# Kernel optimization log

Hardware: AMD Instinct MI355X
Metric: run time of the kernel (lower is better)

## Reference

```python
import jax, jax.numpy as jnp
import numpy as np

N_NODES = 100000


def sage_conv(x, edge_index, Wl, bl, Wr):
    # PyG SAGEConv (aggr='mean', root_weight=True):
    #   out_i = lin_l(mean_{j in N(i)} x_j) + lin_r(x_i)
    src, dst = edge_index[0], edge_index[1]
    msgs = x[src]  # [E, C] gather of source-node features
    summed = jax.ops.segment_sum(msgs, dst, num_segments=N_NODES)
    deg = jax.ops.segment_sum(jnp.ones((edge_index.shape[1],), x.dtype), dst,
                              num_segments=N_NODES)
    mean = summed / jnp.maximum(deg, 1.0)[:, None]  # zero rows stay zero
    return mean @ Wl.T + bl + x @ Wr.T


def setup_inputs() -> dict:
    key = jax.random.key(0)
    ks = jax.random.split(key, 12)
    IN, HID, OUT = 128, 128, 64
    E, P = 1600000, 200000
    x = jax.random.normal(ks[0], (N_NODES, IN), jnp.float32)
    edge_index = jax.random.randint(ks[1], (2, E), 0, N_NODES)
    edge_label_index = jax.random.randint(ks[2], (2, P), 0, N_NODES)
    s1 = 1.0 / np.sqrt(IN)
    s2 = 1.0 / np.sqrt(HID)
    s3 = 1.0 / np.sqrt(2 * OUT)
    return {
        "x": x,
        "edge_index": edge_index,
        "edge_label_index": edge_label_index,
        "Wl1": jax.random.uniform(ks[3], (HID, IN), jnp.float32, -s1, s1),
        "bl1": jnp.zeros((HID,), jnp.float32),
        "Wr1": jax.random.uniform(ks[4], (HID, IN), jnp.float32, -s1, s1),
        "Wl2": jax.random.uniform(ks[5], (OUT, HID), jnp.float32, -s2, s2),
        "bl2": jnp.zeros((OUT,), jnp.float32),
        "Wr2": jax.random.uniform(ks[6], (OUT, HID), jnp.float32, -s2, s2),
        "Wdec": jax.random.uniform(ks[7], (1, 2 * OUT), jnp.float32, -s3, s3),
        "bdec": jax.random.uniform(ks[8], (1,), jnp.float32, -s3, s3),
    }


def reference(x, edge_index, edge_label_index, Wl1, bl1, Wr1, Wl2, bl2, Wr2,
              Wdec, bdec):
    # encode: SAGEConv -> relu -> (dropout p=0) -> SAGEConv
    h = jax.nn.relu(sage_conv(x, edge_index, Wl1, bl1, Wr1))
    z = sage_conv(h, edge_index, Wl2, bl2, Wr2)
    # decode: gather endpoint embeddings, concat, linear -> [P]
    feats = jnp.concatenate([z[edge_label_index[0]], z[edge_label_index[1]]],
                            axis=-1)
    return (feats @ Wdec.T + bdec).reshape(-1)
```

## Files before the change

### kernel.cpp

```cpp
#include <hip/hip_runtime.h>

#define NN 100000
#define NBUK ((NN + 255) / 256)
#define BCAP 5120

typedef unsigned short u16;
typedef unsigned int u32;
typedef __attribute__((ext_vector_type(8))) short short8v;
typedef __attribute__((ext_vector_type(4))) float float4v;

__device__ __forceinline__ u32 f2bf_rne(float f) {
    u32 x = __float_as_uint(f);
    return (x + 0x7fffu + ((x >> 16) & 1u)) >> 16;
}
__device__ __forceinline__ float bf2f(u32 u) {
    return __uint_as_float(u << 16);
}
__device__ __forceinline__ uint4 pack8u(const float4& a, const float4& b) {
    uint4 u;
    u.x = f2bf_rne(a.x) | (f2bf_rne(a.y) << 16);
    u.y = f2bf_rne(a.z) | (f2bf_rne(a.w) << 16);
    u.z = f2bf_rne(b.x) | (f2bf_rne(b.y) << 16);
    u.w = f2bf_rne(b.z) | (f2bf_rne(b.w) << 16);
    return u;
}

__global__ void zero_buckets_kernel(int* __restrict__ p) {
    int i = threadIdx.x;
    if (i < NBUK) p[i] = 0;
}

__global__ __launch_bounds__(256) void partition_kernel(const int* __restrict__ edges,
                                                        int* __restrict__ bucketCnt,
                                                        int* __restrict__ bucketed, int E) {
    __shared__ int h[NBUK];
    __shared__ int base[NBUK];
    for (int i = threadIdx.x; i < NBUK; i += 256) h[i] = 0;
    __syncthreads();
    int b0 = blockIdx.x * 4096;
    for (int k = threadIdx.x; k < 4096; k += 256) {
        int e = b0 + k;
        if (e < E) atomicAdd(&h[edges[E + e] >> 8], 1);
    }
    __syncthreads();
    for (int i = threadIdx.x; i < NBUK; i += 256) {
        int c = h[i];
        base[i] = c ? (i * BCAP + atomicAdd(&bucketCnt[i], c)) : 0;
        h[i] = 0;
    }
    __syncthreads();
    for (int k = threadIdx.x; k < 4096; k += 256) {
        int e = b0 + k;
        if (e < E) {
            int d = edges[E + e];
            int b = d >> 8;
            int off = atomicAdd(&h[b], 1);
            bucketed[base[b] + off] = edges[e] | ((d & 255) << 20);
        }
    }
}

__global__ __launch_bounds__(256) void bucket_sort_kernel(const int* __restrict__ bucketed,
                                                          const int* __restrict__ bucketCnt,
                                                          int* __restrict__ rowStart,
                                                          int* __restrict__ cnt,
                                                          int* __restrict__ sortedSrc, int N) {
    __shared__ int h[256];
    __shared__ int pos[256];
    int b = blockIdx.x;
    int tid = threadIdx.x;
    int start = b * BCAP, end = start + bucketCnt[b];
    h[tid] = 0;
    __syncthreads();
    for (int k = start + tid; k < end; k += 256) atomicAdd(&h[bucketed[k] >> 20], 1);
    __syncthreads();
    int v = h[tid];
    pos[tid] = v;
    __syncthreads();
    for (int off = 1; off < 256; off <<= 1) {
        int t = (tid >= off) ? pos[tid - off] : 0;
        __syncthreads();
        pos[tid] += t;
        __syncthreads();
    }
    int excl = start + pos[tid] - v;
    int node = (b << 8) + tid;
    if (node < N) {
        rowStart[node] = excl;
        cnt[node] = v;
    }
    h[tid] = excl;
    __syncthreads();
    for (int k = start + tid; k < end; k += 256) {
        int entry = bucketed[k];
        int p = atomicAdd(&h[entry >> 20], 1);
        sortedSrc[p] = entry & 0xFFFFF;
    }
}

template <bool XF32>
__global__ __launch_bounds__(256, 2) void gemm_mfma_kernel(
    const void* __restrict__ Xv, const float* __restrict__ Wa,
    const float* __restrict__ Wb, int CHALF,
    u16* __restrict__ Ob, int OSTRIDE, int N)
{
    __shared__ u16 As[128 * 128];

    const int tid = threadIdx.x;
    const int w = tid >> 6;
    const int l = tid & 63;
    const int l15 = l & 15;
    const int lhi = l >> 4;
    const int rowBase = blockIdx.x * 128;
    const int cBase = blockIdx.y * 128;
    char* asb = reinterpret_cast<char*>(As);

#pragma unroll
    for (int i = 0; i < 8; ++i) {
        int q = tid + i * 256;
        int r = q >> 4, c = q & 15;
        int gr = rowBase + r;
        uint4 pk = make_uint4(0u, 0u, 0u, 0u);
        if (gr < N) {
            if (XF32) {
                const float* xf = (const float*)Xv + (size_t)gr * 128 + c * 8;
                float4 f0 = *reinterpret_cast<const float4*>(xf);
                float4 f1 = *reinterpret_cast<const float4*>(xf + 4);
                pk = pack8u(f0, f1);
            } else {
                pk = *reinterpret_cast<const uint4*>((const u16*)Xv + (size_t)gr * 128 + c * 8);
            }
        }
        *reinterpret_cast<uint4*>(asb + r * 256 + ((c * 16) ^ ((r & 7) << 4))) = pk;
    }

    short8v bfrag[2][4];
#pragma unroll
    for (int nj = 0; nj < 2; ++nj) {
        int c = cBase + w * 32 + nj * 16 + l15;
        const float* wr = (c < CHALF) ? (Wa + (size_t)c * 128)
                                      : (Wb + (size_t)(c - CHALF) * 128);
#pragma unroll
        for (int kk = 0; kk < 4; ++kk) {
            float4 f0 = *reinterpret_cast<const float4*>(wr + kk * 32 + lhi * 8);
            float4 f1 = *reinterpret_cast<const float4*>(wr + kk * 32 + lhi * 8 + 4);
            uint4 pk = pack8u(f0, f1);
            union { uint4 u; short8v s; } cv; cv.u = pk;
            bfrag[nj][kk] = cv.s;
        }
    }

    __syncthreads();

    float4v acc[8][2];
    const float4v az = {0.f, 0.f, 0.f, 0.f};
#pragma unroll
    for (int mi = 0; mi < 8; ++mi) { acc[mi][0] = az; acc[mi][1] = az; }

#pragma unroll
    for (int kk = 0; kk < 4; ++kk) {
#pragma unroll
        for (int mi = 0; mi < 8; ++mi) {
            int r = mi * 16 + l15;
            short8v a = *reinterpret_cast<const short8v*>(
                asb + r * 256 + ((kk * 64 + lhi * 16) ^ ((r & 7) << 4)));
            acc[mi][0] = __builtin_amdgcn_mfma_f32_16x16x32_bf16(a, bfrag[0][kk], acc[mi][0], 0, 0, 0);
            acc[mi][1] = __builtin_amdgcn_mfma_f32_16x16x32_bf16(a, bfrag[1][kk], acc[mi][1], 0, 0, 0);
        }
    }

    __syncthreads();
#pragma unroll
    for (int mi = 0; mi < 8; ++mi) {
#pragma unroll
        for (int nj = 0; nj < 2; ++nj) {
            int cc = w * 32 + nj * 16 + l15;
#pragma unroll
            for (int j = 0; j < 4; ++j) {
                int r = mi * 16 + lhi * 4 + j;
                *reinterpret_cast<u16*>(asb + r * 256 + ((cc * 2) ^ ((r & 7) << 4)))
                    = (u16)f2bf_rne(acc[mi][nj][j]);
            }
        }
    }
    __syncthreads();
#pragma unroll
    for (int i = 0; i < 8; ++i) {
        int q = tid + i * 256;
        int r = q >> 4, c = q & 15;
        int gr = rowBase + r;
        if (gr < N) {
            uint4 v = *reinterpret_cast<const uint4*>(
                asb + r * 256 + ((c * 16) ^ ((r & 7) << 4)));
            *reinterpret_cast<uint4*>(&Ob[(size_t)gr * OSTRIDE + cBase + c * 8]) = v;
        }
    }
}

template <int C, bool RELU>
__global__ __launch_bounds__(256) void agg_combine_kernel(
    const u16* __restrict__ T, int tStride,
    const u16* __restrict__ R,
    const int* __restrict__ sortedSrc, const int* __restrict__ rowStart,
    const int* __restrict__ cnt, const float* __restrict__ bias,
    u16* __restrict__ outB, int N)
{
    constexpr int TPN = C / 8;
    constexpr int NPB = 256 / TPN;
    int n = blockIdx.x * NPB + threadIdx.x / TPN;
    int c = threadIdx.x % TPN;
    if (n >= N) return;
    int start = rowStart[n];
    int m = cnt[n];
    const int* __restrict__ ep = sortedSrc + start;
    const u16* __restrict__ tp = T + c * 8;

    float a0 = 0.f, a1 = 0.f, a2 = 0.f, a3 = 0.f;
    float a4 = 0.f, a5 = 0.f, a6 = 0.f, a7 = 0.f;
    int k = 0;
    for (; k + 8 <= m; k += 8) {
        int s[8];
        uint4 v[8];
#pragma unroll
        for (int u = 0; u < 8; ++u) s[u] = ep[k + u];
#pragma unroll
        for (int u = 0; u < 8; ++u)
            v[u] = *reinterpret_cast<const uint4*>(&tp[(size_t)s[u] * tStride]);
#pragma unroll
        for (int h = 0; h < 2; ++h) {
            const uint4& w0 = v[h * 4 + 0]; const uint4& w1 = v[h * 4 + 1];
            const uint4& w2 = v[h * 4 + 2]; const uint4& w3 = v[h * 4 + 3];
            a0 += bf2f(w0.x & 0xffffu) + bf2f(w1.x & 0xffffu) + bf2f(w2.x & 0xffffu) + bf2f(w3.x & 0xffffu);
            a1 += bf2f(w0.x >> 16) + bf2f(w1.x >> 16) + bf2f(w2.x >> 16) + bf2f(w3.x >> 16);
            a2 += bf2f(w0.y & 0xffffu) + bf2f(w1.y & 0xffffu) + bf2f(w2.y & 0xffffu) + bf2f(w3.y & 0xffffu);
            a3 += bf2f(w0.y >> 16) + bf2f(w1.y >> 16) + bf2f(w2.y >> 16) + bf2f(w3.y >> 16);
            a4 += bf2f(w0.z & 0xffffu) + bf2f(w1.z & 0xffffu) + bf2f(w2.z & 0xffffu) + bf2f(w3.z & 0xffffu);
            a5 += bf2f(w0.z >> 16) + bf2f(w1.z >> 16) + bf2f(w2.z >> 16) + bf2f(w3.z >> 16);
            a6 += bf2f(w0.w & 0xffffu) + bf2f(w1.w & 0xffffu) + bf2f(w2.w & 0xffffu) + bf2f(w3.w & 0xffffu);
            a7 += bf2f(w0.w >> 16) + bf2f(w1.w >> 16) + bf2f(w2.w >> 16) + bf2f(w3.w >> 16);
        }
    }
    for (; k + 4 <= m; k += 4) {
        int s0 = ep[k], s1 = ep[k + 1], s2 = ep[k + 2], s3 = ep[k + 3];
        uint4 w0 = *reinterpret_cast<const uint4*>(&tp[(size_t)s0 * tStride]);
        uint4 w1 = *reinterpret_cast<const uint4*>(&tp[(size_t)s1 * tStride]);
        uint4 w2 = *reinterpret_cast<const uint4*>(&tp[(size_t)s2 * tStride]);
        uint4 w3 = *reinterpret_cast<const uint4*>(&tp[(size_t)s3 * tStride]);
        a0 += bf2f(w0.x & 0xffffu) + bf2f(w1.x & 0xffffu) + bf2f(w2.x & 0xffffu) + bf2f(w3.x & 0xffffu);
        a1 += bf2f(w0.x >> 16) + bf2f(w1.x >> 16) + bf2f(w2.x >> 16) + bf2f(w3.x >> 16);
        a2 += bf2f(w0.y & 0xffffu) + bf2f(w1.y & 0xffffu) + bf2f(w2.y & 0xffffu) + bf2f(w3.y & 0xffffu);
        a3 += bf2f(w0.y >> 16) + bf2f(w1.y >> 16) + bf2f(w2.y >> 16) + bf2f(w3.y >> 16);
        a4 += bf2f(w0.z & 0xffffu) + bf2f(w1.z & 0xffffu) + bf2f(w2.z & 0xffffu) + bf2f(w3.z & 0xffffu);
        a5 += bf2f(w0.z >> 16) + bf2f(w1.z >> 16) + bf2f(w2.z >> 16) + bf2f(w3.z >> 16);
        a6 += bf2f(w0.w & 0xffffu) + bf2f(w1.w & 0xffffu) + bf2f(w2.w & 0xffffu) + bf2f(w3.w & 0xffffu);
        a7 += bf2f(w0.w >> 16) + bf2f(w1.w >> 16) + bf2f(w2.w >> 16) + bf2f(w3.w >> 16);
    }
    for (; k < m; ++k) {
        uint4 v = *reinterpret_cast<const uint4*>(&tp[(size_t)ep[k] * tStride]);
        a0 += bf2f(v.x & 0xffffu); a1 += bf2f(v.x >> 16);
        a2 += bf2f(v.y & 0xffffu); a3 += bf2f(v.y >> 16);
        a4 += bf2f(v.z & 0xffffu); a5 += bf2f(v.z >> 16);
        a6 += bf2f(v.w & 0xffffu); a7 += bf2f(v.w >> 16);
    }
    float inv = 1.0f / fmaxf((float)m, 1.0f);
    uint4 rv = *reinterpret_cast<const uint4*>(&R[(size_t)n * tStride + c * 8]);
    float o0 = fmaf(a0, inv, bias[c * 8 + 0]) + bf2f(rv.x & 0xffffu);
    float o1 = fmaf(a1, inv, bias[c * 8 + 1]) + bf2f(rv.x >> 16);
    float o2 = fmaf(a2, inv, bias[c * 8 + 2]) + bf2f(rv.y & 0xffffu);
    float o3 = fmaf(a3, inv, bias[c * 8 + 3]) + bf2f(rv.y >> 16);
    float o4 = fmaf(a4, inv, bias[c * 8 + 4]) + bf2f(rv.z & 0xffffu);
    float o5 = fmaf(a5, inv, bias[c * 8 + 5]) + bf2f(rv.z >> 16);
    float o6 = fmaf(a6, inv, bias[c * 8 + 6]) + bf2f(rv.w & 0xffffu);
    float o7 = fmaf(a7, inv, bias[c * 8 + 7]) + bf2f(rv.w >> 16);
    if (RELU) {
        o0 = fmaxf(o0, 0.f); o1 = fmaxf(o1, 0.f);
        o2 = fmaxf(o2, 0.f); o3 = fmaxf(o3, 0.f);
        o4 = fmaxf(o4, 0.f); o5 = fmaxf(o5, 0.f);
        o6 = fmaxf(o6, 0.f); o7 = fmaxf(o7, 0.f);
    }
    uint4 o;
    o.x = f2bf_rne(o0) | (f2bf_rne(o1) << 16);
    o.y = f2bf_rne(o2) | (f2bf_rne(o3) << 16);
    o.z = f2bf_rne(o4) | (f2bf_rne(o5) << 16);
    o.w = f2bf_rne(o6) | (f2bf_rne(o7) << 16);
    *reinterpret_cast<uint4*>(&outB[(size_t)n * C + c * 8]) = o;
}

__global__ __launch_bounds__(256) void decode_kernel(
    const u16* __restrict__ z, const int* __restrict__ eli,
    const float* __restrict__ Wdec, const float* __restrict__ bdec,
    float* __restrict__ out, int P)
{
    int t = blockIdx.x * 256 + threadIdx.x;
    int p = t >> 6;
    int lane = t & 63;
    if (p >= P) return;
    int a = eli[p];
    int b = eli[P + p];
    float acc = bf2f(z[(size_t)a * 64 + lane]) * Wdec[lane]
              + bf2f(z[(size_t)b * 64 + lane]) * Wdec[64 + lane];
    for (int off = 32; off; off >>= 1) acc += __shfl_down(acc, off);
    if (lane == 0) out[p] = acc + bdec[0];
}

extern "C" void kernel_launch(void* const* d_in, const int* in_sizes, int n_in,
                              void* d_out, int out_size, void* d_ws, size_t ws_size,
                              hipStream_t stream) {
    const float* x    = (const float*)d_in[0];
    const int*   ei   = (const int*)d_in[1];
    const int*   eli  = (const int*)d_in[2];
    const float* Wl1  = (const float*)d_in[3];
    const float* bl1  = (const float*)d_in[4];
    const float* Wr1  = (const float*)d_in[5];
    const float* Wl2  = (const float*)d_in[6];
    const float* bl2  = (const float*)d_in[7];
    const float* Wr2  = (const float*)d_in[8];
    const float* Wdec = (const float*)d_in[9];
    const float* bdec = (const float*)d_in[10];
    float* out = (float*)d_out;

    const int N = NN;
    const int E = in_sizes[1] / 2;
    const int P = in_sizes[2] / 2;
    const int EB = (E + 4095) / 4096;

    char* wp = (char*)d_ws;
    u16* obf = (u16*)wp;  wp += (size_t)N * 256 * 2;
    u16* hbf = (u16*)wp;  wp += (size_t)N * 128 * 2;
    u16* zb  = (u16*)wp;  wp += (size_t)N * 64 * 2;
    int* bucketCnt = (int*)wp;
    int* rowStart  = bucketCnt + NBUK;
    int* cnt       = rowStart + N;
    int* bucketed  = cnt + N;
    int* sortedSrc = bucketed + NBUK * BCAP;

    zero_buckets_kernel<<<1, 512, 0, stream>>>(bucketCnt);
    partition_kernel<<<EB, 256, 0, stream>>>(ei, bucketCnt, bucketed, E);
    bucket_sort_kernel<<<NBUK, 256, 0, stream>>>(bucketed, bucketCnt, rowStart, cnt, sortedSrc, N);

    {
        dim3 grid((N + 127) / 128, 2);
        gemm_mfma_kernel<true><<<grid, 256, 0, stream>>>(x, Wl1, Wr1, 128, obf, 256, N);
    }
    agg_combine_kernel<128, true><<<(N + 15) / 16, 256, 0, stream>>>(
        obf, 256, obf + 128, sortedSrc, rowStart, cnt, bl1, hbf, N);

    {
        dim3 grid((N + 127) / 128, 1);
        gemm_mfma_kernel<false><<<grid, 256, 0, stream>>>(hbf, Wl2, Wr2, 64, obf, 128, N);
    }
    agg_combine_kernel<64, false><<<(N + 31) / 32, 256, 0, stream>>>(
        obf, 128, obf + 64, sortedSrc, rowStart, cnt, bl2, zb, N);

    decode_kernel<<<(P + 3) / 4, 256, 0, stream>>>(zb, eli, Wdec, bdec, out, P);
}
```

Before: 233.4 us.

## Fold decoder into second aggregation and loop column blocks inside GEMM

The second-layer aggregation now projects each node's z straight onto the two halves of the decoder weights and stores a per-node float2 (u, v), so decode only gathers two floats per label pair instead of two 64-wide bf16 rows. The first-layer GEMM loops over both 128-column blocks inside one workgroup, reusing the staged A tile instead of launching a second grid column that reloads and reconverts x. It adds a separate LDS output buffer for this. The zero-init kernel is replaced by hipMemsetAsync, and the 4-wide remainder loop in aggregation is dropped. The trade-offs are more LDS per block (lower occupancy) and a different bf16 rounding point, since z is no longer stored as bf16 before the decoder.

After: 210.9 us. -9.6%, faster.

```diff
diff --git a/kernel.cpp b/kernel.cpp
--- a/kernel.cpp
+++ b/kernel.cpp
@@ -23,11 +23,6 @@
     u.z = f2bf_rne(b.x) | (f2bf_rne(b.y) << 16);
     u.w = f2bf_rne(b.z) | (f2bf_rne(b.w) << 16);
     return u;
-}
-
-__global__ void zero_buckets_kernel(int* __restrict__ p) {
-    int i = threadIdx.x;
-    if (i < NBUK) p[i] = 0;
 }
 
 __global__ __launch_bounds__(256) void partition_kernel(const int* __restrict__ edges,
@@ -98,13 +93,14 @@
     }
 }
 
-template <bool XF32>
+template <bool XF32, int NCB>
 __global__ __launch_bounds__(256, 2) void gemm_mfma_kernel(
     const void* __restrict__ Xv, const float* __restrict__ Wa,
     const float* __restrict__ Wb, int CHALF,
     u16* __restrict__ Ob, int OSTRIDE, int N)
 {
     __shared__ u16 As[128 * 128];
+    __shared__ u16 Cs[128 * 128];
 
     const int tid = threadIdx.x;
     const int w = tid >> 6;
@@ -112,8 +108,8 @@
     const int l15 = l & 15;
     const int lhi = l >> 4;
     const int rowBase = blockIdx.x * 128;
-    const int cBase = blockIdx.y * 128;
     char* asb = reinterpret_cast<char*>(As);
+    char* csb = reinterpret_cast<char*>(Cs);
 
 #pragma unroll
     for (int i = 0; i < 8; ++i) {
@@ -133,66 +129,68 @@
         }
         *reinterpret_cast<uint4*>(asb + r * 256 + ((c * 16) ^ ((r & 7) << 4))) = pk;
     }
-
-    short8v bfrag[2][4];
-#pragma unroll
-    for (int nj = 0; nj < 2; ++nj) {
-        int c = cBase + w * 32 + nj * 16 + l15;
-        const float* wr = (c < CHALF) ? (Wa + (size_t)c * 128)
-                                      : (Wb + (size_t)(c - CHALF) * 128);
+    __syncthreads();
+
+    for (int cb = 0; cb < NCB; ++cb) {
+        const int cBase = cb * 128;
+        short8v bfrag[2][4];
+#pragma unroll
+        for (int nj = 0; nj < 2; ++nj) {
+            int c = cBase + w * 32 + nj * 16 + l15;
+            const float* wr = (c < CHALF) ? (Wa + (size_t)c * 128)
+                                          : (Wb + (size_t)(c - CHALF) * 128);
+#pragma unroll
+            for (int kk = 0; kk < 4; ++kk) {
+                float4 f0 = *reinterpret_cast<const float4*>(wr + kk * 32 + lhi * 8);
+                float4 f1 = *reinterpret_cast<const float4*>(wr + kk * 32 + lhi * 8 + 4);
+                uint4 pk = pack8u(f0, f1);
+                union { uint4 u; short8v s; } cv; cv.u = pk;
+                bfrag[nj][kk] = cv.s;
+            }
+        }
+
+        float4v acc[8][2];
+        const float4v az = {0.f, 0.f, 0.f, 0.f};
+#pragma unroll
+        for (int mi = 0; mi < 8; ++mi) { acc[mi][0] = az; acc[mi][1] = az; }
+
 #pragma unroll
         for (int kk = 0; kk < 4; ++kk) {
-            float4 f0 = *reinterpret_cast<const float4*>(wr + kk * 32 + lhi * 8);
-            float4 f1 = *reinterpret_cast<const float4*>(wr + kk * 32 + lhi * 8 + 4);
-            uint4 pk = pack8u(f0, f1);
-            union { uint4 u; short8v s; } cv; cv.u = pk;
-            bfrag[nj][kk] = cv.s;
-        }
-    }
-
-    __syncthreads();
-
-    float4v acc[8][2];
-    const float4v az = {0.f, 0.f, 0.f, 0.f};
-#pragma unroll
-    for (int mi = 0; mi < 8; ++mi) { acc[mi][0] = az; acc[mi][1] = az; }
-
-#pragma unroll
-    for (int kk = 0; kk < 4; ++kk) {
+#pragma unroll
+            for (int mi = 0; mi < 8; ++mi) {
+                int r = mi * 16 + l15;
+                short8v a = *reinterpret_cast<const short8v*>(
+                    asb + r * 256 + ((kk * 64 + lhi * 16) ^ ((r & 7) << 4)));
+                acc[mi][0] = __builtin_amdgcn_mfma_f32_16x16x32_bf16(a, bfrag[0][kk], acc[mi][0], 0, 0, 0);
+                acc[mi][1] = __builtin_amdgcn_mfma_f32_16x16x32_bf16(a, bfrag[1][kk], acc[mi][1], 0, 0, 0);
+            }
+        }
+
+        if (cb) __syncthreads();
 #pragma unroll
         for (int mi = 0; mi < 8; ++mi) {
-            int r = mi * 16 + l15;
-            short8v a = *reinterpret_cast<const short8v*>(
-                asb + r * 256 + ((kk * 64 + lhi * 16) ^ ((r & 7) << 4)));
-            acc[mi][0] = __builtin_amdgcn_mfma_f32_16x16x32_bf16(a, bfrag[0][kk], acc[mi][0], 0, 0, 0);
-            acc[mi][1] = __builtin_amdgcn_mfma_f32_16x16x32_bf16(a, bfrag[1][kk], acc[mi][1], 0, 0, 0);
-        }
-    }
-
-    __syncthreads();
-#pragma unroll
-    for (int mi = 0; mi < 8; ++mi) {
-#pragma unroll
-        for (int nj = 0; nj < 2; ++nj) {
-            int cc = w * 32 + nj * 16 + l15;
-#pragma unroll
-            for (int j = 0; j < 4; ++j) {
-                int r = mi * 16 + lhi * 4 + j;
-                *reinterpret_cast<u16*>(asb + r * 256 + ((cc * 2) ^ ((r & 7) << 4)))
-                    = (u16)f2bf_rne(acc[mi][nj][j]);
+#pragma unroll
+            for (int nj = 0; nj < 2; ++nj) {
+                int cc = w * 32 + nj * 16 + l15;
+#pragma unroll
+                for (int j = 0; j < 4; ++j) {
+                    int r = mi * 16 + lhi * 4 + j;
+                    *reinterpret_cast<u16*>(csb + r * 256 + ((cc * 2) ^ ((r & 7) << 4)))
+                        = (u16)f2bf_rne(acc[mi][nj][j]);
+                }
             }
         }
-    }
-    __syncthreads();
-#pragma unroll
-    for (int i = 0; i < 8; ++i) {
-        int q = tid + i * 256;
-        int r = q >> 4, c = q & 15;
-        int gr = rowBase + r;
-        if (gr < N) {
-            uint4 v = *reinterpret_cast<const uint4*>(
-                asb + r * 256 + ((c * 16) ^ ((r & 7) << 4)));
-            *reinterpret_cast<uint4*>(&Ob[(size_t)gr * OSTRIDE + cBase + c * 8]) = v;
+        __syncthreads();
+#pragma unroll
+        for (int i = 0; i < 8; ++i) {
+            int q = tid + i * 256;
+            int r = q >> 4, c = q & 15;
+            int gr = rowBase + r;
+            if (gr < N) {
+                uint4 v = *reinterpret_cast<const uint4*>(
+                    csb + r * 256 + ((c * 16) ^ ((r & 7) << 4)));
+                *reinterpret_cast<uint4*>(&Ob[(size_t)gr * OSTRIDE + cBase + c * 8]) = v;
+            }
         }
     }
 }
@@ -240,21 +238,6 @@
             a7 += bf2f(w0.w >> 16) + bf2f(w1.w >> 16) + bf2f(w2.w >> 16) + bf2f(w3.w >> 16);
         }
     }
-    for (; k + 4 <= m; k += 4) {
-        int s0 = ep[k], s1 = ep[k + 1], s2 = ep[k + 2], s3 = ep[k + 3];
-        uint4 w0 = *reinterpret_cast<const uint4*>(&tp[(size_t)s0 * tStride]);
-        uint4 w1 = *reinterpret_cast<const uint4*>(&tp[(size_t)s1 * tStride]);
-        uint4 w2 = *reinterpret_cast<const uint4*>(&tp[(size_t)s2 * tStride]);
-        uint4 w3 = *reinterpret_cast<const uint4*>(&tp[(size_t)s3 * tStride]);
-        a0 += bf2f(w0.x & 0xffffu) + bf2f(w1.x & 0xffffu) + bf2f(w2.x & 0xffffu) + bf2f(w3.x & 0xffffu);
-        a1 += bf2f(w0.x >> 16) + bf2f(w1.x >> 16) + bf2f(w2.x >> 16) + bf2f(w3.x >> 16);
-        a2 += bf2f(w0.y & 0xffffu) + bf2f(w1.y & 0xffffu) + bf2f(w2.y & 0xffffu) + bf2f(w3.y & 0xffffu);
-        a3 += bf2f(w0.y >> 16) + bf2f(w1.y >> 16) + bf2f(w2.y >> 16) + bf2f(w3.y >> 16);
-        a4 += bf2f(w0.z & 0xffffu) + bf2f(w1.z & 0xffffu) + bf2f(w2.z & 0xffffu) + bf2f(w3.z & 0xffffu);
-        a5 += bf2f(w0.z >> 16) + bf2f(w1.z >> 16) + bf2f(w2.z >> 16) + bf2f(w3.z >> 16);
-        a6 += bf2f(w0.w & 0xffffu) + bf2f(w1.w & 0xffffu) + bf2f(w2.w & 0xffffu) + bf2f(w3.w & 0xffffu);
-        a7 += bf2f(w0.w >> 16) + bf2f(w1.w >> 16) + bf2f(w2.w >> 16) + bf2f(w3.w >> 16);
-    }
     for (; k < m; ++k) {
         uint4 v = *reinterpret_cast<const uint4*>(&tp[(size_t)ep[k] * tStride]);
         a0 += bf2f(v.x & 0xffffu); a1 += bf2f(v.x >> 16);
@@ -286,21 +269,89 @@
     *reinterpret_cast<uint4*>(&outB[(size_t)n * C + c * 8]) = o;
 }
 
+__global__ __launch_bounds__(256) void agg_uv_kernel(
+    const u16* __restrict__ T, int tStride,
+    const u16* __restrict__ R,
+    const int* __restrict__ sortedSrc, const int* __restrict__ rowStart,
+    const int* __restrict__ cnt, const float* __restrict__ bias,
+    const float* __restrict__ Wdec, float2* __restrict__ uv, int N)
+{
+    constexpr int TPN = 8;
+    constexpr int NPB = 256 / TPN;
+    int n = blockIdx.x * NPB + threadIdx.x / TPN;
+    int c = threadIdx.x % TPN;
+    if (n >= N) return;
+    int start = rowStart[n];
+    int m = cnt[n];
+    const int* __restrict__ ep = sortedSrc + start;
+    const u16* __restrict__ tp = T + c * 8;
+
+    float a0 = 0.f, a1 = 0.f, a2 = 0.f, a3 = 0.f;
+    float a4 = 0.f, a5 = 0.f, a6 = 0.f, a7 = 0.f;
+    int k = 0;
+    for (; k + 8 <= m; k += 8) {
+        int s[8];
+        uint4 v[8];
+#pragma unroll
+        for (int u = 0; u < 8; ++u) s[u] = ep[k + u];
+#pragma unroll
+        for (int u = 0; u < 8; ++u)
+            v[u] = *reinterpret_cast<const uint4*>(&tp[(size_t)s[u] * tStride]);
+#pragma unroll
+        for (int h = 0; h < 2; ++h) {
+            const uint4& w0 = v[h * 4 + 0]; const uint4& w1 = v[h * 4 + 1];
+            const uint4& w2 = v[h * 4 + 2]; const uint4& w3 = v[h * 4 + 3];
+            a0 += bf2f(w0.x & 0xffffu) + bf2f(w1.x & 0xffffu) + bf2f(w2.x & 0xffffu) + bf2f(w3.x & 0xffffu);
+            a1 += bf2f(w0.x >> 16) + bf2f(w1.x >> 16) + bf2f(w2.x >> 16) + bf2f(w3.x >> 16);
+            a2 += bf2f(w0.y & 0xffffu) + bf2f(w1.y & 0xffffu) + bf2f(w2.y & 0xffffu) + bf2f(w3.y & 0xffffu);
+            a3 += bf2f(w0.y >> 16) + bf2f(w1.y >> 16) + bf2f(w2.y >> 16) + bf2f(w3.y >> 16);
+            a4 += bf2f(w0.z & 0xffffu) + bf2f(w1.z & 0xffffu) + bf2f(w2.z & 0xffffu) + bf2f(w3.z & 0xffffu);
+            a5 += bf2f(w0.z >> 16) + bf2f(w1.z >> 16) + bf2f(w2.z >> 16) + bf2f(w3.z >> 16);
+            a6 += bf2f(w0.w & 0xffffu) + bf2f(w1.w & 0xffffu) + bf2f(w2.w & 0xffffu) + bf2f(w3.w & 0xffffu);
+            a7 += bf2f(w0.w >> 16) + bf2f(w1.w >> 16) + bf2f(w2.w >> 16) + bf2f(w3.w >> 16);
+        }
+    }
+    for (; k < m; ++k) {
+        uint4 v = *reinterpret_cast<const uint4*>(&tp[(size_t)ep[k] * tStride]);
+        a0 += bf2f(v.x & 0xffffu); a1 += bf2f(v.x >> 16);
+        a2 += bf2f(v.y & 0xffffu); a3 += bf2f(v.y >> 16);
+        a4 += bf2f(v.z & 0xffffu); a5 += bf2f(v.z >> 16);
+        a6 += bf2f(v.w & 0xffffu); a7 += bf2f(v.w >> 16);
+    }
+    float inv = 1.0f / fmaxf((float)m, 1.0f);
+    uint4 rv = *reinterpret_cast<const uint4*>(&R[(size_t)n * tStride + c * 8]);
+    float z0 = fmaf(a0, inv, bias[c * 8 + 0]) + bf2f(rv.x & 0xffffu);
+    float z1 = fmaf(a1, inv, bias[c * 8 + 1]) + bf2f(rv.x >> 16);
+    float z2 = fmaf(a2, inv, bias[c * 8 + 2]) + bf2f(rv.y & 0xffffu);
+    float z3 = fmaf(a3, inv, bias[c * 8 + 3]) + bf2f(rv.y >> 16);
+    float z4 = fmaf(a4, inv, bias[c * 8 + 4]) + bf2f(rv.z & 0xffffu);
+    float z5 = fmaf(a5, inv, bias[c * 8 + 5]) + bf2f(rv.z >> 16);
+    float z6 = fmaf(a6, inv, bias[c * 8 + 6]) + bf2f(rv.w & 0xffffu);
+    float z7 = fmaf(a7, inv, bias[c * 8 + 7]) + bf2f(rv.w >> 16);
+
+    const float* wu = Wdec + c * 8;
+    const float* wv = Wdec + 64 + c * 8;
+    float u = z0 * wu[0] + z1 * wu[1] + z2 * wu[2] + z3 * wu[3]
+            + z4 * wu[4] + z5 * wu[5] + z6 * wu[6] + z7 * wu[7];
+    float v = z0 * wv[0] + z1 * wv[1] + z2 * wv[2] + z3 * wv[3]
+            + z4 * wv[4] + z5 * wv[5] + z6 * wv[6] + z7 * wv[7];
+#pragma unroll
+    for (int mk = 4; mk; mk >>= 1) {
+        u += __shfl_xor(u, mk, 8);
+        v += __shfl_xor(v, mk, 8);
+    }
+    if (c == 0) uv[n] = make_float2(u, v);
+}
+
 __global__ __launch_bounds__(256) void decode_kernel(
-    const u16* __restrict__ z, const int* __restrict__ eli,
-    const float* __restrict__ Wdec, const float* __restrict__ bdec,
-    float* __restrict__ out, int P)
+    const float2* __restrict__ uv, const int* __restrict__ eli,
+    const float* __restrict__ bdec, float* __restrict__ out, int P)
 {
-    int t = blockIdx.x * 256 + threadIdx.x;
-    int p = t >> 6;
-    int lane = t & 63;
+    int p = blockIdx.x * 256 + threadIdx.x;
     if (p >= P) return;
     int a = eli[p];
     int b = eli[P + p];
-    float acc = bf2f(z[(size_t)a * 64 + lane]) * Wdec[lane]
-              + bf2f(z[(size_t)b * 64 + lane]) * Wdec[64 + lane];
-    for (int off = 32; off; off >>= 1) acc += __shfl_down(acc, off);
-    if (lane == 0) out[p] = acc + bdec[0];
+    out[p] = uv[a].x + uv[b].y + bdec[0];
 }
 
 extern "C" void kernel_launch(void* const* d_in, const int* in_sizes, int n_in,
@@ -327,30 +378,26 @@
     char* wp = (char*)d_ws;
     u16* obf = (u16*)wp;  wp += (size_t)N * 256 * 2;
     u16* hbf = (u16*)wp;  wp += (size_t)N * 128 * 2;
-    u16* zb  = (u16*)wp;  wp += (size_t)N * 64 * 2;
+    float2* uv = (float2*)wp; wp += (size_t)N * 8;
     int* bucketCnt = (int*)wp;
     int* rowStart  = bucketCnt + NBUK;
     int* cnt       = rowStart + N;
     int* bucketed  = cnt + N;
     int* sortedSrc = bucketed + NBUK * BCAP;
 
-    zero_buckets_kernel<<<1, 512, 0, stream>>>(bucketCnt);
+    hipMemsetAsync(bucketCnt, 0, NBUK * sizeof(int), stream);
     partition_kernel<<<EB, 256, 0, stream>>>(ei, bucketCnt, bucketed, E);
     bucket_sort_kernel<<<NBUK, 256, 0, stream>>>(bucketed, bucketCnt, rowStart, cnt, sortedSrc, N);
 
-    {
-        dim3 grid((N + 127) / 128, 2);
-        gemm_mfma_kernel<true><<<grid, 256, 0, stream>>>(x, Wl1, Wr1, 128, obf, 256, N);
-    }
+    gemm_mfma_kernel<true, 2><<<(N + 127) / 128, 256, 0, stream>>>(
+        x, Wl1, Wr1, 128, obf, 256, N);
     agg_combine_kernel<128, true><<<(N + 15) / 16, 256, 0, stream>>>(
         obf, 256, obf + 128, sortedSrc, rowStart, cnt, bl1, hbf, N);
 
-    {
-        dim3 grid((N + 127) / 128, 1);
-        gemm_mfma_kernel<false><<<grid, 256, 0, stream>>>(hbf, Wl2, Wr2, 64, obf, 128, N);
-    }
-    agg_combine_kernel<64, false><<<(N + 31) / 32, 256, 0, stream>>>(
-        obf, 128, obf + 64, sortedSrc, rowStart, cnt, bl2, zb, N);
-
-    decode_kernel<<<(P + 3) / 4, 256, 0, stream>>>(zb, eli, Wdec, bdec, out, P);
-}
+    gemm_mfma_kernel<false, 1><<<(N + 127) / 128, 256, 0, stream>>>(
+        hbf, Wl2, Wr2, 64, obf, 128, N);
+    agg_uv_kernel<<<(N + 31) / 32, 256, 0, stream>>>(
+        obf, 128, obf + 64, sortedSrc, rowStart, cnt, bl2, Wdec, uv, N);
+
+    decode_kernel<<<(P + 255) / 256, 256, 0, stream>>>(uv, eli, bdec, out, P);
+}
```
